# Performance work log

Hardware: AMD Instinct MI355X
Metric: run time of the kernel (lower is better)

The kernel has to match this reference:

```python
import jax, jax.numpy as jnp
import numpy as np

EPS = 1e-12  # F.normalize default eps


def _l2_normalize(v, axis):
    n = jnp.sqrt(jnp.sum(v * v, axis=axis, keepdims=True))
    return v / jnp.maximum(n, EPS)


def setup_inputs() -> dict:
    key = jax.random.key(0)
    k1, k2, k3 = jax.random.split(key, 3)
    N, D, H, W, K = 64, 256, 64, 64, 64
    x = jax.random.normal(k1, (N, D, H, W), dtype=jnp.float32)
    conv_w = jax.random.normal(k2, (K, D), dtype=jnp.float32) * 0.05  # 1x1 conv weight (K,D,1,1) squeezed
    centroids = jax.random.uniform(k3, (K, D), dtype=jnp.float32)    # torch.rand init
    return {"x": x, "conv_w": conv_w, "centroids": centroids}


def reference(x, conv_w, centroids):
    N, D, H, W = x.shape
    K = conv_w.shape[0]
    # normalize_input: L2 normalize across channel dim
    x = _l2_normalize(x, axis=1)
    xf = x.reshape(N, D, H * W)                      # [N, D, T]
    # 1x1 conv == per-pixel matmul with (K, D) weight
    logits = jnp.einsum('kd,ndt->nkt', conv_w, xf)    # [N, K, T]
    a = jax.nn.softmax(logits, axis=1)                # softmax over clusters
    # vlad[n,k,d] = sum_t a[n,k,t] * (xf[n,d,t] - c[k,d])
    #            = (a @ xf^T)[n,k,d] - (sum_t a[n,k,t]) * c[k,d]
    vlad = jnp.einsum('nkt,ndt->nkd', a, xf) - a.sum(axis=-1)[..., None] * centroids
    vlad = _l2_normalize(vlad, axis=2)                # intra-normalization
    flat = vlad.reshape(N, K * D)
    return _l2_normalize(flat, axis=1)                # final L2 norm
```

## Files before the change

### kernel.cpp

```cpp
#include <hip/hip_runtime.h>

#define FEPS 1e-12f

typedef __attribute__((ext_vector_type(8))) short short8;
typedef __attribute__((ext_vector_type(4))) short bf16x4;
typedef __attribute__((ext_vector_type(4))) float floatx4;

constexpr int NB = 64, D = 256, T = 4096, K = 64, S = 8;
constexpr int TC = 64;
constexpr int TBLK = T / S;
constexpr int NCH = TBLK / TC;

__device__ __forceinline__ unsigned short f2bf(float f) {
    unsigned u = __float_as_uint(f);
    return (unsigned short)((u + 0x7FFFu + ((u >> 16) & 1u)) >> 16);
}
__device__ __forceinline__ unsigned pk2(float a, float b) {
    return (unsigned)f2bf(a) | ((unsigned)f2bf(b) << 16);
}

__device__ __forceinline__ void barrier_nd() {
    __builtin_amdgcn_sched_barrier(0);
    asm volatile("s_waitcnt lgkmcnt(0)" ::: "memory");
    __builtin_amdgcn_s_barrier();
    __builtin_amdgcn_sched_barrier(0);
}

__global__ __launch_bounds__(512, 2)
void nv_main(const float* __restrict__ x, const float* __restrict__ w,
             float* __restrict__ vout, float* __restrict__ suma)
{
    __shared__ __align__(16) unsigned char smem[76800];
    unsigned short* bmm = (unsigned short*)(smem + 65536);
    float* sps = (float*)(smem + 73728);
    float* sqp = (float*)(smem + 74752);
    float* fb  = (float*)smem;

    const int tid = threadIdx.x;
    const int wv = tid >> 6, ln = tid & 63;
    const int m = ln & 15, g = ln >> 4;
    const int a = wv & 3, b = wv >> 2;
    const int bid = blockIdx.x;
    const int n = (bid & 7) * 8 + ((bid >> 3) & 7);
    const int ts = bid >> 6;

    const float* xn = x + (size_t)n * D * T;

    short8 wf[8];
    {
        const float* wp = w + (16 * a + m) * D + 8 * g;
        #pragma unroll
        for (int ks = 0; ks < 8; ++ks) {
            float4 q0 = *(const float4*)(wp + 32 * ks);
            float4 q1 = *(const float4*)(wp + 32 * ks + 4);
            union { short8 v; unsigned u[4]; } t_;
            t_.u[0] = pk2(q0.x, q0.y); t_.u[1] = pk2(q0.z, q0.w);
            t_.u[2] = pk2(q1.x, q1.y); t_.u[3] = pk2(q1.z, q1.w);
            wf[ks] = t_.v;
        }
    }

    floatx4 acc[4][2];
    floatx4 fzero = {0.f, 0.f, 0.f, 0.f};
    #pragma unroll
    for (int p = 0; p < 4; ++p) { acc[p][0] = fzero; acc[p][1] = fzero; }
    float sa[4] = {0.f, 0.f, 0.f, 0.f};

    float4 pvA[4], pvB[4];
    float4 sq4;

    auto issueH = [&](float4* pv, int cc, int s0) {
        const int tn = ts * TBLK + cc * TC;
        #pragma unroll
        for (int s = 0; s < 4; ++s)
            pv[s] = *(const float4*)(
                xn + (size_t)(32 * wv + 4 * (s0 + s) + g) * T + tn + 4 * m);
    };
    auto stageH = [&](const float4* pv, int bufsel, int s0) {
        #pragma unroll
        for (int s = 0; s < 4; ++s) {
            float4 v = pv[s];
            sq4.x = fmaf(v.x, v.x, sq4.x); sq4.y = fmaf(v.y, v.y, sq4.y);
            sq4.z = fmaf(v.z, v.z, sq4.z); sq4.w = fmaf(v.w, v.w, sq4.w);
            uint2 st2; st2.x = pk2(v.x, v.y); st2.y = pk2(v.z, v.w);
            const int dd = 4 * (s0 + s) + g;
            *(uint2*)(smem + bufsel * 32768 + wv * 4096 + (m >> 2) * 1024
                      + dd * 32 + (m & 3) * 8) = st2;
        }
    };
    auto sqzero = [&]() {
        sq4.x = 0.f; sq4.y = 0.f; sq4.z = 0.f; sq4.w = 0.f;
    };
    auto sqreduce = [&]() {
        #pragma unroll
        for (int msk = 16; msk <= 32; msk <<= 1) {
            sq4.x += __shfl_xor(sq4.x, msk); sq4.y += __shfl_xor(sq4.y, msk);
            sq4.z += __shfl_xor(sq4.z, msk); sq4.w += __shfl_xor(sq4.w, msk);
        }
        if (g == 0) {
            sqp[(4 * m + 0) * 8 + wv] = sq4.x;
            sqp[(4 * m + 1) * 8 + wv] = sq4.y;
            sqp[(4 * m + 2) * 8 + wv] = sq4.z;
            sqp[(4 * m + 3) * 8 + wv] = sq4.w;
        }
    };

    issueH(pvA, 0, 0); issueH(pvB, 0, 4);
    sqzero();
    stageH(pvA, 0, 0); stageH(pvB, 0, 4);
    sqreduce();

    for (int c = 0; c < NCH; ++c) {
        const int cur = c & 1;
        barrier_nd();

        if (c + 1 < NCH) issueH(pvA, c + 1, 0);

        float r4[2];
        #pragma unroll
        for (int nt = 0; nt < 2; ++nt) {
            const int t = 32 * b + 16 * nt + m;
            float4 p0 = *(const float4*)(&sqp[t * 8]);
            float4 p1 = *(const float4*)(&sqp[t * 8 + 4]);
            float ss = ((p0.x + p0.y) + (p0.z + p0.w))
                     + ((p1.x + p1.y) + (p1.z + p1.w));
            r4[nt] = 1.f / fmaxf(sqrtf(ss), FEPS);
        }
        asm volatile("s_waitcnt lgkmcnt(0)" ::: "memory");
        __builtin_amdgcn_sched_barrier(0);

        floatx4 z[2];
        z[0] = fzero; z[1] = fzero;
        const int trb = cur * 32768 + 2048 * b + 256 * g + 2 * m;
        bf16x4 hb[2][2][2];
        {
            asm volatile("ds_read_b64_tr_b16 %0, %2 offset:0\n\t"
                         "ds_read_b64_tr_b16 %1, %2 offset:128"
                         : "=&v"(hb[0][0][0]), "=&v"(hb[0][0][1])
                         : "v"(trb));
            asm volatile("ds_read_b64_tr_b16 %0, %2 offset:0\n\t"
                         "ds_read_b64_tr_b16 %1, %2 offset:128"
                         : "=&v"(hb[0][1][0]), "=&v"(hb[0][1][1])
                         : "v"(trb + 1024));
        }
        #pragma unroll
        for (int ks = 0; ks < 8; ++ks) {
            const int pc = ks & 1;
            if (ks < 7) {
                const int an = trb + (ks + 1) * 4096;
                asm volatile("ds_read_b64_tr_b16 %0, %2 offset:0\n\t"
                             "ds_read_b64_tr_b16 %1, %2 offset:128"
                             : "=&v"(hb[pc ^ 1][0][0]), "=&v"(hb[pc ^ 1][0][1])
                             : "v"(an));
                asm volatile("ds_read_b64_tr_b16 %0, %2 offset:0\n\t"
                             "ds_read_b64_tr_b16 %1, %2 offset:128"
                             : "=&v"(hb[pc ^ 1][1][0]), "=&v"(hb[pc ^ 1][1][1])
                             : "v"(an + 1024));
                asm volatile("s_waitcnt lgkmcnt(4)" ::: "memory");
            } else {
                asm volatile("s_waitcnt lgkmcnt(0)" ::: "memory");
            }
            __builtin_amdgcn_sched_barrier(0);
            #pragma unroll
            for (int nt = 0; nt < 2; ++nt) {
                short8 bfr = __builtin_shufflevector(
                    hb[pc][nt][0], hb[pc][nt][1], 0, 1, 2, 3, 4, 5, 6, 7);
                z[nt] = __builtin_amdgcn_mfma_f32_16x16x32_bf16(
                    wf[ks], bfr, z[nt], 0, 0, 0);
            }
        }

        if (c + 1 < NCH) issueH(pvB, c + 1, 4);

        float e[2][4], psum[2];
        #pragma unroll
        for (int nt = 0; nt < 2; ++nt) {
            const float r = r4[nt];
            float p = 0.f;
            #pragma unroll
            for (int reg = 0; reg < 4; ++reg) {
                float ex = __expf(z[nt][reg] * r);
                e[nt][reg] = ex; p += ex;
            }
            psum[nt] = p;
        }
        #pragma unroll
        for (int nt = 0; nt < 2; ++nt) {
            psum[nt] += __shfl_xor(psum[nt], 16);
            psum[nt] += __shfl_xor(psum[nt], 32);
        }
        if (g == 0) {
            #pragma unroll
            for (int nt = 0; nt < 2; ++nt)
                sps[(32 * b + 16 * nt + m) * 4 + a] = psum[nt];
        }
        barrier_nd();
        #pragma unroll
        for (int nt = 0; nt < 2; ++nt) {
            const int t = 32 * b + 16 * nt + m;
            float4 sv = *(const float4*)(&sps[t * 4]);
            const float inv = 1.f / (sv.x + sv.y + sv.z + sv.w);
            const float br = inv * r4[nt];
            #pragma unroll
            for (int reg = 0; reg < 4; ++reg) {
                const int k = 16 * a + 4 * g + reg;
                bmm[k * TC + (t ^ (8 * (k & 7)))] = f2bf(e[nt][reg] * br);
                sa[reg] += e[nt][reg] * inv;
            }
        }

        sqzero();
        if (c + 1 < NCH) stageH(pvA, cur ^ 1, 0);
        barrier_nd();

        #pragma unroll
        for (int kt = 0; kt < 2; ++kt) {
            short8 bf[2];
            #pragma unroll
            for (int nt2 = 0; nt2 < 2; ++nt2)
                bf[nt2] = *(const short8*)(smem + cur * 32768 + wv * 4096
                           + (2 * kt + (g >> 1)) * 1024
                           + (16 * nt2 + m) * 32 + (g & 1) * 16);
            #pragma unroll
            for (int mt = 0; mt < 4; ++mt) {
                const int k = 16 * mt + m;
                short8 af = *(const short8*)(
                    &bmm[k * TC + ((32 * kt + 8 * g) ^ (8 * (k & 7)))]);
                #pragma unroll
                for (int nt2 = 0; nt2 < 2; ++nt2)
                    acc[mt][nt2] = __builtin_amdgcn_mfma_f32_16x16x32_bf16(
                        af, bf[nt2], acc[mt][nt2], 0, 0, 0);
            }
        }

        if (c + 1 < NCH) { stageH(pvB, cur ^ 1, 4); sqreduce(); }
    }

    barrier_nd();
    #pragma unroll
    for (int mt = 0; mt < 4; ++mt)
        #pragma unroll
        for (int nt2 = 0; nt2 < 2; ++nt2)
            #pragma unroll
            for (int reg = 0; reg < 4; ++reg)
                fb[(16 * mt + 4 * g + reg) * D + 32 * wv + 16 * nt2 + m] =
                    acc[mt][nt2][reg];
    barrier_nd();
    {
        float* vs = vout + (size_t)n * K * D;
        #pragma unroll
        for (int j = 0; j < 32; ++j) {
            const int off = wv * 2048 + j * 64 + ln;
            atomicAdd(&vs[off], fb[off]);
        }
    }
    #pragma unroll
    for (int reg = 0; reg < 4; ++reg) {
        float v = sa[reg];
        v += __shfl_xor(v, 1); v += __shfl_xor(v, 2);
        v += __shfl_xor(v, 4); v += __shfl_xor(v, 8);
        if (m == 0) atomicAdd(&suma[n * K + 16 * a + 4 * g + reg], v);
    }
}

__global__ void nv_finish_row(const float* __restrict__ cent,
                              const float* __restrict__ suma,
                              float* __restrict__ out)
{
    const int bid = blockIdx.x;
    const int k = bid & 63;
    const int d = threadIdx.x;
    float v = out[(size_t)bid * D + d] - suma[bid] * cent[k * D + d];
    float sv = v * v;
    #pragma unroll
    for (int msk = 1; msk < 64; msk <<= 1) sv += __shfl_xor(sv, msk);
    __shared__ float red[4];
    __shared__ float stot;
    if ((d & 63) == 0) red[d >> 6] = sv;
    __syncthreads();
    if (d == 0) stot = red[0] + red[1] + red[2] + red[3];
    __syncthreads();
    const float inv = 0.125f / fmaxf(sqrtf(stot), FEPS);
    out[(size_t)bid * D + d] = v * inv;
}

extern "C" void kernel_launch(void* const* d_in, const int* in_sizes, int n_in,
                              void* d_out, int out_size, void* d_ws, size_t ws_size,
                              hipStream_t stream)
{
    const float* x    = (const float*)d_in[0];
    const float* w    = (const float*)d_in[1];
    const float* cent = (const float*)d_in[2];
    float* out = (float*)d_out;

    float* suma = (float*)d_ws;

    (void)hipMemsetAsync(d_ws, 0, (size_t)NB * K * sizeof(float), stream);
    (void)hipMemsetAsync(d_out, 0, (size_t)NB * K * D * sizeof(float), stream);

    nv_main<<<S * NB, 512, 0, stream>>>(x, w, out, suma);
    nv_finish_row<<<NB * K, 256, 0, stream>>>(cent, suma, out);
}
```

Baseline: 97.19 us.

## Fuse row normalization into main kernel via last-block completion counter

Removes the separate finish kernel. Each sample now has an atomic counter, and the last of its S blocks to finish subtracts the centroid term and applies intra-normalization in place. This saves one kernel launch and a second pass over the output. In exchange, the last block for each sample serializes that tail work, and correctness now depends on the fence and atomic-counter ordering.

```diff
diff --git a/kernel.cpp b/kernel.cpp
--- a/kernel.cpp
+++ b/kernel.cpp
@@ -28,13 +28,16 @@
 
 __global__ __launch_bounds__(512, 2)
 void nv_main(const float* __restrict__ x, const float* __restrict__ w,
-             float* __restrict__ vout, float* __restrict__ suma)
+             const float* __restrict__ cent,
+             float* __restrict__ vout, float* __restrict__ suma,
+             int* __restrict__ cnt)
 {
     __shared__ __align__(16) unsigned char smem[76800];
     unsigned short* bmm = (unsigned short*)(smem + 65536);
     float* sps = (float*)(smem + 73728);
     float* sqp = (float*)(smem + 74752);
     float* fb  = (float*)smem;
+    __shared__ int lastflag;
 
     const int tid = threadIdx.x;
     const int wv = tid >> 6, ln = tid & 63;
@@ -246,13 +249,11 @@
                 fb[(16 * mt + 4 * g + reg) * D + 32 * wv + 16 * nt2 + m] =
                     acc[mt][nt2][reg];
     barrier_nd();
-    {
-        float* vs = vout + (size_t)n * K * D;
-        #pragma unroll
-        for (int j = 0; j < 32; ++j) {
-            const int off = wv * 2048 + j * 64 + ln;
-            atomicAdd(&vs[off], fb[off]);
-        }
+    float* vs = vout + (size_t)n * K * D;
+    #pragma unroll
+    for (int j = 0; j < 32; ++j) {
+        const int off = wv * 2048 + j * 64 + ln;
+        atomicAdd(&vs[off], fb[off]);
     }
     #pragma unroll
     for (int reg = 0; reg < 4; ++reg) {
@@ -261,27 +262,36 @@
         v += __shfl_xor(v, 4); v += __shfl_xor(v, 8);
         if (m == 0) atomicAdd(&suma[n * K + 16 * a + 4 * g + reg], v);
     }
-}
-
-__global__ void nv_finish_row(const float* __restrict__ cent,
-                              const float* __restrict__ suma,
-                              float* __restrict__ out)
-{
-    const int bid = blockIdx.x;
-    const int k = bid & 63;
-    const int d = threadIdx.x;
-    float v = out[(size_t)bid * D + d] - suma[bid] * cent[k * D + d];
-    float sv = v * v;
-    #pragma unroll
-    for (int msk = 1; msk < 64; msk <<= 1) sv += __shfl_xor(sv, msk);
-    __shared__ float red[4];
-    __shared__ float stot;
-    if ((d & 63) == 0) red[d >> 6] = sv;
+
+    __threadfence();
+    if (tid == 0) lastflag = (atomicAdd(&cnt[n], 1) == S - 1) ? 1 : 0;
     __syncthreads();
-    if (d == 0) stot = red[0] + red[1] + red[2] + red[3];
-    __syncthreads();
-    const float inv = 0.125f / fmaxf(sqrtf(stot), FEPS);
-    out[(size_t)bid * D + d] = v * inv;
+    if (lastflag) {
+        __threadfence();
+        #pragma unroll
+        for (int r = 0; r < 8; ++r) {
+            const int row = wv * 8 + r;
+            const float sm = __hip_atomic_load(&suma[n * K + row],
+                                __ATOMIC_RELAXED, __HIP_MEMORY_SCOPE_AGENT);
+            float v0[4];
+            float sv = 0.f;
+            #pragma unroll
+            for (int j = 0; j < 4; ++j) {
+                const int idx = row * D + 64 * j + ln;
+                float val = __hip_atomic_load(&vs[idx],
+                                __ATOMIC_RELAXED, __HIP_MEMORY_SCOPE_AGENT);
+                v0[j] = val - sm * cent[row * D + 64 * j + ln];
+                sv = fmaf(v0[j], v0[j], sv);
+            }
+            #pragma unroll
+            for (int msk = 1; msk < 64; msk <<= 1)
+                sv += __shfl_xor(sv, msk);
+            const float inv = 0.125f / fmaxf(sqrtf(sv), FEPS);
+            #pragma unroll
+            for (int j = 0; j < 4; ++j)
+                vs[row * D + 64 * j + ln] = v0[j] * inv;
+        }
+    }
 }
 
 extern "C" void kernel_launch(void* const* d_in, const int* in_sizes, int n_in,
@@ -294,10 +304,10 @@
     float* out = (float*)d_out;
 
     float* suma = (float*)d_ws;
-
-    (void)hipMemsetAsync(d_ws, 0, (size_t)NB * K * sizeof(float), stream);
+    int*   cnt  = (int*)((char*)d_ws + (size_t)NB * K * sizeof(float));
+
+    (void)hipMemsetAsync(d_ws, 0, (size_t)(NB * K + NB) * 4, stream);
     (void)hipMemsetAsync(d_out, 0, (size_t)NB * K * D * sizeof(float), stream);
 
-    nv_main<<<S * NB, 512, 0, stream>>>(x, w, out, suma);
-    nv_finish_row<<<NB * K, 256, 0, stream>>>(cent, suma, out);
-}
+    nv_main<<<S * NB, 512, 0, stream>>>(x, w, cent, out, suma, cnt);
+}
```

New measurement: 152.2 us. 56.6% more time.
